# Optimization experiments

Hardware: AMD Instinct MI355X
Metric: run time of the kernel (lower is better)

## Reference

```python
import jax, jax.numpy as jnp
import numpy as np

# ---- constants derived from init kwargs ----
XB = (-30.0, 30.0, 0.15); YB = (-15.0, 15.0, 0.15)
NX = np.array([(XB[1]-XB[0])/XB[2], (YB[1]-YB[0])/YB[2]], np.float32)   # [400, 200]
DX = np.array([XB[2], YB[2]], np.float32)
BX = np.array([XB[0]+XB[2]/2.0, YB[0]+YB[2]/2.0], np.float32)
BOUND = DX/2.0 - BX                                                      # [30, 15]
CDIST_THR = float(np.linalg.norm(1.5/(2.0*BOUND)))
NUM_CLASSES = 3
B, N, G, PTS_PER_INS = 16, 1024, 1024, 32


def setup_inputs() -> dict:
    key = jax.random.key(0)
    k1, k2, k3, k4, k5 = jax.random.split(key, 5)
    # matches/semantics are log-probs (NLLLoss expects log-space inputs)
    matches = jax.nn.log_softmax(jax.random.normal(k1, (B, N+1, N+1), jnp.float32), axis=-1)
    positions = jax.random.uniform(k2, (B, N, 2), jnp.float32) * (jnp.asarray(NX) - 1.0)
    semantics = jax.nn.log_softmax(jax.random.normal(k3, (B, NUM_CLASSES, N), jnp.float32), axis=1)
    masks = jnp.ones((B, N, 1), jnp.float32)
    # raw GT points in metric coords in [-bound, bound]
    gt_pts = (jax.random.uniform(k4, (B, G, 2), jnp.float32) * 2.0 - 1.0) * jnp.asarray(BOUND)
    gt_ins = jnp.broadcast_to(jnp.arange(G, dtype=jnp.int32) // PTS_PER_INS, (B, G))
    gt_order = jnp.broadcast_to(jnp.arange(G, dtype=jnp.int32) % PTS_PER_INS, (B, G))
    gt_type = jax.random.randint(k5, (B, G), 0, NUM_CLASSES, dtype=jnp.int32)
    return {"matches": matches, "positions": positions, "semantics": semantics,
            "masks": masks, "gt_pts": gt_pts, "gt_ins": gt_ins,
            "gt_order": gt_order, "gt_type": gt_type}


def _per_sample(match, position, semantic, gt_pts, gt_ins, gt_order, gt_type):
    nx = jnp.asarray(NX, position.dtype)
    bound = jnp.asarray(BOUND, position.dtype)
    n = position.shape[0]
    pos = position / (nx - 1.0)                        # [N,2] normalized preds
    pgt = (gt_pts + bound) / (2.0 * bound)             # [G,2] normalized GT
    # cdist pred->gt, nearest GT per prediction
    cd = jnp.sqrt(jnp.sum((pos[:, None, :] - pgt[None, :, :])**2, -1) + 1e-12)  # [N,G]
    nearest = jnp.argmin(cd, 1)                        # [N]
    ndist = jnp.min(cd, 1)
    ins = jnp.where(ndist < CDIST_THR, gt_ins[nearest], -1)   # instance id or -1
    order = gt_order[nearest]
    # group preds by instance, sort by within-instance order (stable by index),
    # connect consecutive members: match_gt[prev, next] = 1
    perm = jnp.lexsort((jnp.arange(n), order, ins))    # primary key = ins
    a, b = perm[:-1], perm[1:]
    same = (ins[a] == ins[b]) & (ins[a] >= 0)
    M = jnp.zeros((n + 1, n + 1), match.dtype)
    M = M.at[a, b].add(same.astype(match.dtype))       # (a,b) pairs are unique
    # conflict resolution: each column keeps only the closest (in pred space) row
    dist_map = jnp.sqrt(jnp.sum((pos[:, None, :] - pos[None, :, :])**2, -1) + 1e-12)  # [N,N]
    blk = M[:n, :n]
    colsum = blk.sum(0)
    best = jnp.argmin(jnp.where(blk > 0, dist_map, jnp.inf), 0)             # [N]
    newblk = jax.nn.one_hot(best, n, dtype=match.dtype).T * (colsum > 0)    # [N,N]
    M = M.at[:n, :n].set(newblk)
    # dustbin assignments for unmatched rows/cols
    rowsum = M[:n, :].sum(1)
    M = M.at[:n, n].set((rowsum == 0).astype(match.dtype))
    colsum2 = M[:, :n].sum(0)
    M = M.at[n, :n].set((colsum2 == 0).astype(match.dtype))
    # NLL match losses (forward/backward direction), dustbin row/col excluded from targets
    t_back = jnp.argmax(M, 0)[:n]                      # per column: matched row
    t_fwd = jnp.argmax(M, 1)[:n]                       # per row: matched col
    j = jnp.arange(n)
    mloss = -jnp.mean(match[j, t_fwd]) - jnp.mean(match[j, t_back])
    # semantic gt from nearest GT type (no distance threshold, as in original)
    sem_cls = gt_type[nearest]                         # [N]
    sg = jax.nn.one_hot(sem_cls, NUM_CLASSES, dtype=semantic.dtype).T   # [C,N]
    semloss = -jnp.mean(semantic[sem_cls, j])
    closs = jnp.mean(jnp.abs(pos - pgt[nearest]))
    return closs, mloss, semloss, M, sg


def reference(matches, positions, semantics, masks, gt_pts, gt_ins, gt_order, gt_type):
    # masks assumed all-ones (full validity), so boolean compaction is identity
    closs, mloss, semloss, matches_gt, semantics_gt = jax.vmap(_per_sample)(
        matches, positions, semantics, gt_pts, gt_ins, gt_order, gt_type)
    return (jnp.mean(closs), jnp.mean(mloss), jnp.mean(semloss), matches_gt, semantics_gt)
```

## Files before the change

kernel.cpp:

```cpp
#include <hip/hip_runtime.h>
#include <math.h>

#define BB 16
#define NN 1024
#define GG 1024
#define NP1 1025
#define NC 3

__device__ __forceinline__ void get_consts(float& bnd0, float& bnd1,
                                           float& tb0, float& tb1, float& thr) {
    const float bx0 = (float)(-30.0 + 0.15 / 2.0);
    const float bx1 = (float)(-15.0 + 0.15 / 2.0);
    bnd0 = __fsub_rn(__fmul_rn(0.15f, 0.5f), bx0);
    bnd1 = __fsub_rn(__fmul_rn(0.15f, 0.5f), bx1);
    tb0 = __fmul_rn(2.0f, bnd0); tb1 = __fmul_rn(2.0f, bnd1);
    const float q0 = __fdiv_rn(1.5f, tb0), q1 = __fdiv_rn(1.5f, tb1);
    thr = __fsqrt_rn(__fadd_rn(__fmul_rn(q0, q0), __fmul_rn(q1, q1)));
}

__global__ void k_zero(float* __restrict__ out) {
    const long long idx = (long long)blockIdx.x * blockDim.x + threadIdx.x;
    const long long T   = (long long)gridDim.x * blockDim.x;
    float4* f4 = (float4*)(out + 4);
    const long long n4 = (16810000LL - 1) / 4;
    float4 z; z.x = 0.f; z.y = 0.f; z.z = 0.f; z.w = 0.f;
    for (long long k = idx; k < n4; k += T) f4[k] = z;
    if (idx == 0) {
        out[3] = 0.f;
        out[16810000] = 0.f; out[16810001] = 0.f; out[16810002] = 0.f;
    }
}

__global__ __launch_bounds__(128) void k_nearest1(
    const float* __restrict__ positions, const float* __restrict__ gt_pts,
    unsigned long long* __restrict__ part)
{
    __shared__ float2 sp[128];
    const int b = blockIdx.y;
    const int pc = blockIdx.x & 7, gs = blockIdx.x >> 3;
    const int tid = threadIdx.x;
    float bnd0, bnd1, tb0, tb1, thr;
    get_consts(bnd0, bnd1, tb0, tb1, thr);

    {
        const int g = (gs << 7) + tid;
        float2 gp = ((const float2*)gt_pts)[b * GG + g];
        float2 pg;
        pg.x = __fdiv_rn(__fadd_rn(gp.x, bnd0), tb0);
        pg.y = __fdiv_rn(__fadd_rn(gp.y, bnd1), tb1);
        sp[tid] = pg;
    }
    __syncthreads();

    const int i = (pc << 7) + tid;
    float2 p = ((const float2*)positions)[b * NN + i];
    const float px = __fdiv_rn(p.x, 399.0f);
    const float py = __fdiv_rn(p.y, 199.0f);

    unsigned long long best = ~0ull;
    const int gbase = gs << 7;
    #pragma unroll 8
    for (int g = 0; g < 128; ++g) {
        float2 pg = sp[g];
        float dx = __fsub_rn(px, pg.x);
        float dy = __fsub_rn(py, pg.y);
        float s  = __fadd_rn(__fadd_rn(__fmul_rn(dx, dx), __fmul_rn(dy, dy)), 1e-12f);
        float cd = __fsqrt_rn(s);
        unsigned long long pk =
            ((unsigned long long)__float_as_uint(cd) << 10) | (unsigned)(gbase + g);
        best = (pk < best) ? pk : best;
    }
    part[(((b << 3) + gs) << 10) + i] = best;
}

__global__ __launch_bounds__(128) void k_combine(
    const float* __restrict__ positions, const float* __restrict__ gt_pts,
    const int* __restrict__ gt_ins, const int* __restrict__ gt_order,
    const int* __restrict__ gt_type,
    const unsigned long long* __restrict__ part,
    int* __restrict__ key_ws, int* __restrict__ sem_ws,
    int* __restrict__ tf_ws, int* __restrict__ tb_ws,
    float* __restrict__ closs_part)
{
    __shared__ float red[128];
    const int b = blockIdx.y, pc = blockIdx.x, tid = threadIdx.x;
    const int i = (pc << 7) + tid;
    float bnd0, bnd1, tb0, tb1, thr;
    get_consts(bnd0, bnd1, tb0, tb1, thr);

    unsigned long long best = part[((b << 3) << 10) + i];
    #pragma unroll
    for (int gs = 1; gs < 8; ++gs) {
        unsigned long long v = part[(((b << 3) + gs) << 10) + i];
        best = (v < best) ? v : best;
    }
    const int bi = (int)(best & 1023u);
    const float cd = __uint_as_float((unsigned)(best >> 10));

    const int ins = (cd < thr) ? gt_ins[b * GG + bi] : -1;
    const int key = ((ins + 1) << 15) | (gt_order[b * GG + bi] << 10) | i;
    key_ws[(b << 10) + i] = key;
    sem_ws[(b << 10) + i] = gt_type[b * GG + bi];
    tf_ws[(b << 10) + i] = NN;
    tb_ws[(b << 10) + i] = NN;

    float2 p = ((const float2*)positions)[b * NN + i];
    const float px = __fdiv_rn(p.x, 399.0f);
    const float py = __fdiv_rn(p.y, 199.0f);
    float2 gp = ((const float2*)gt_pts)[b * GG + bi];
    const float pgx = __fdiv_rn(__fadd_rn(gp.x, bnd0), tb0);
    const float pgy = __fdiv_rn(__fadd_rn(gp.y, bnd1), tb1);
    const float cl = fabsf(__fsub_rn(px, pgx)) + fabsf(__fsub_rn(py, pgy));

    red[tid] = cl; __syncthreads();
    for (int s = 64; s > 0; s >>= 1) {
        if (tid < s) red[tid] += red[tid + s];
        __syncthreads();
    }
    if (tid == 0) closs_part[(b << 3) + pc] = red[0];
}

__global__ __launch_bounds__(128) void k_rank(
    const int* __restrict__ key_ws, int* __restrict__ sorted_ws)
{
    __shared__ int sk[NN];
    const int b = blockIdx.y, pc = blockIdx.x, tid = threadIdx.x;
    for (int j = tid; j < NN; j += 128) sk[j] = key_ws[(b << 10) + j];
    __syncthreads();
    const int k = sk[(pc << 7) + tid];
    int rank = 0;
    const int4* sk4 = (const int4*)sk;
    #pragma unroll 8
    for (int j = 0; j < 256; ++j) {
        int4 v = sk4[j];
        rank += (v.x < k) + (v.y < k) + (v.z < k) + (v.w < k);
    }
    sorted_ws[(b << 10) + rank] = k;
}

__global__ __launch_bounds__(128) void k_edges(
    const int* __restrict__ sorted_ws,
    int* __restrict__ tf_ws, int* __restrict__ tb_ws)
{
    const int b = blockIdx.y;
    const int p = (blockIdx.x << 7) + threadIdx.x;
    if (p >= NN - 1) return;
    const int k0 = sorted_ws[(b << 10) + p];
    const int k1 = sorted_ws[(b << 10) + p + 1];
    const int ia = (k0 >> 15) - 1;
    const int ic = (k1 >> 15) - 1;
    if (ia == ic && ia >= 0) {
        const int a = k0 & 1023, c = k1 & 1023;
        tf_ws[(b << 10) + a] = c;
        tb_ws[(b << 10) + c] = a;
    }
}

__global__ __launch_bounds__(128) void k_out(
    const float* __restrict__ matches, const float* __restrict__ semantics,
    const int* __restrict__ sem_ws,
    const int* __restrict__ tf_ws, const int* __restrict__ tb_ws,
    float* __restrict__ out, double* __restrict__ mpart, double* __restrict__ spart)
{
    __shared__ double redm[128], reds[128];
    const int b = blockIdx.y, pc = blockIdx.x, tid = threadIdx.x;
    const int i = (pc << 7) + tid;

    const int jf = tf_ws[(b << 10) + i];
    const int jb = tb_ws[(b << 10) + i];

    float* Mb = out + 3 + (size_t)b * NP1 * NP1;
    Mb[(size_t)i * NP1 + jf] = 1.0f;
    if (jb == NN) Mb[(size_t)NN * NP1 + i] = 1.0f;

    const float* mrow = matches + (size_t)b * NP1 * NP1 + (size_t)i * NP1;
    const double mp = (double)mrow[jf] + (double)mrow[jb];

    const int sc = sem_ws[(b << 10) + i];
    const double sv = (double)semantics[(b * NC + sc) * NN + i];

    float* sg = out + 3 + (size_t)BB * NP1 * NP1 + (size_t)b * NC * NN;
    sg[0 * NN + i] = (sc == 0) ? 1.0f : 0.0f;
    sg[1 * NN + i] = (sc == 1) ? 1.0f : 0.0f;
    sg[2 * NN + i] = (sc == 2) ? 1.0f : 0.0f;

    redm[tid] = mp; reds[tid] = sv; __syncthreads();
    for (int s = 64; s > 0; s >>= 1) {
        if (tid < s) { redm[tid] += redm[tid + s]; reds[tid] += reds[tid + s]; }
        __syncthreads();
    }
    if (tid == 0) { mpart[(b << 3) + pc] = redm[0]; spart[(b << 3) + pc] = reds[0]; }
}

__global__ __launch_bounds__(128) void k_final(
    const float* __restrict__ closs_part, const double* __restrict__ mpart,
    const double* __restrict__ spart, float* __restrict__ out)
{
    __shared__ double rc[128], rm[128], rs[128];
    const int t = threadIdx.x;
    rc[t] = (double)closs_part[t]; rm[t] = mpart[t]; rs[t] = spart[t];
    __syncthreads();
    for (int s = 64; s > 0; s >>= 1) {
        if (t < s) { rc[t] += rc[t + s]; rm[t] += rm[t + s]; rs[t] += rs[t + s]; }
        __syncthreads();
    }
    if (t == 0) {
        out[0] = (float)(rc[0] / 32768.0);
        out[1] = (float)(-rm[0] / 16384.0);
        out[2] = (float)(-rs[0] / 16384.0);
    }
}

extern "C" void kernel_launch(void* const* d_in, const int* in_sizes, int n_in,
                              void* d_out, int out_size, void* d_ws, size_t ws_size,
                              hipStream_t stream) {
    const float* matches   = (const float*)d_in[0];
    const float* positions = (const float*)d_in[1];
    const float* semantics = (const float*)d_in[2];
    const float* gt_pts    = (const float*)d_in[4];
    const int*   gt_ins    = (const int*)d_in[5];
    const int*   gt_order  = (const int*)d_in[6];
    const int*   gt_type   = (const int*)d_in[7];
    float* out = (float*)d_out;

    char* ws = (char*)d_ws;
    unsigned long long* part = (unsigned long long*)ws;
    int*    key_ws     = (int*)(ws + (1 << 20));
    int*    sem_ws     = (int*)(ws + (1 << 20) + (1 << 16));
    int*    sorted_ws  = (int*)(ws + (1 << 20) + (2 << 16));
    int*    tf_ws      = (int*)(ws + (1 << 20) + (3 << 16));
    int*    tb_ws      = (int*)(ws + (1 << 20) + (4 << 16));
    float*  closs_part = (float*)(ws + (1 << 20) + (5 << 16));
    double* mpart      = (double*)(ws + (1 << 20) + (5 << 16) + 1024);
    double* spart      = (double*)(ws + (1 << 20) + (5 << 16) + 2048);

    hipLaunchKernelGGL(k_zero,     dim3(2048),    dim3(256), 0, stream, out);
    hipLaunchKernelGGL(k_nearest1, dim3(64, 16),  dim3(128), 0, stream,
                       positions, gt_pts, part);
    hipLaunchKernelGGL(k_combine,  dim3(8, 16),   dim3(128), 0, stream,
                       positions, gt_pts, gt_ins, gt_order, gt_type, part,
                       key_ws, sem_ws, tf_ws, tb_ws, closs_part);
    hipLaunchKernelGGL(k_rank,     dim3(8, 16),   dim3(128), 0, stream, key_ws, sorted_ws);
    hipLaunchKernelGGL(k_edges,    dim3(8, 16),   dim3(128), 0, stream, sorted_ws, tf_ws, tb_ws);
    hipLaunchKernelGGL(k_out,      dim3(8, 16),   dim3(128), 0, stream,
                       matches, semantics, sem_ws, tf_ws, tb_ws, out, mpart, spart);
    hipLaunchKernelGGL(k_final,    dim3(1),       dim3(128), 0, stream,
                       closs_part, mpart, spart, out);
}
```

Baseline: 154.0 us.

## Fuse nearest search with combine and zero-fill output inside k_out

Merges the split nearest-GT search and its combine pass into one kernel that keeps all GT points in shared memory and reduces the eight partial minima in LDS. This removes the 64-bit partial buffer round trip and one launch. The separate whole-output zeroing kernel is dropped; each k_out block now zeroes its own 32 rows of M before scattering the ones, and writes the dustbin row explicitly. This folds the large memset into the scatter pass but adds a block barrier and smaller per-block work.

```diff
diff --git a/kernel.cpp b/kernel.cpp
--- a/kernel.cpp
+++ b/kernel.cpp
@@ -18,41 +18,31 @@
     thr = __fsqrt_rn(__fadd_rn(__fmul_rn(q0, q0), __fmul_rn(q1, q1)));
 }
 
-__global__ void k_zero(float* __restrict__ out) {
-    const long long idx = (long long)blockIdx.x * blockDim.x + threadIdx.x;
-    const long long T   = (long long)gridDim.x * blockDim.x;
-    float4* f4 = (float4*)(out + 4);
-    const long long n4 = (16810000LL - 1) / 4;
-    float4 z; z.x = 0.f; z.y = 0.f; z.z = 0.f; z.w = 0.f;
-    for (long long k = idx; k < n4; k += T) f4[k] = z;
-    if (idx == 0) {
-        out[3] = 0.f;
-        out[16810000] = 0.f; out[16810001] = 0.f; out[16810002] = 0.f;
-    }
-}
-
-__global__ __launch_bounds__(128) void k_nearest1(
+__global__ __launch_bounds__(512) void k_near(
     const float* __restrict__ positions, const float* __restrict__ gt_pts,
-    unsigned long long* __restrict__ part)
-{
-    __shared__ float2 sp[128];
-    const int b = blockIdx.y;
-    const int pc = blockIdx.x & 7, gs = blockIdx.x >> 3;
-    const int tid = threadIdx.x;
+    const int* __restrict__ gt_ins, const int* __restrict__ gt_order,
+    const int* __restrict__ gt_type,
+    int* __restrict__ key_ws, int* __restrict__ sem_ws,
+    int* __restrict__ tf_ws, int* __restrict__ tb_ws,
+    float* __restrict__ closs_part)
+{
+    __shared__ float2 sp[GG];
+    __shared__ unsigned long long pl[512];
+    const int b = blockIdx.y, pc = blockIdx.x, tid = threadIdx.x;
+    const int sub = tid & 63, gs = tid >> 6;
     float bnd0, bnd1, tb0, tb1, thr;
     get_consts(bnd0, bnd1, tb0, tb1, thr);
 
-    {
-        const int g = (gs << 7) + tid;
+    for (int g = tid; g < GG; g += 512) {
         float2 gp = ((const float2*)gt_pts)[b * GG + g];
         float2 pg;
         pg.x = __fdiv_rn(__fadd_rn(gp.x, bnd0), tb0);
         pg.y = __fdiv_rn(__fadd_rn(gp.y, bnd1), tb1);
-        sp[tid] = pg;
-    }
-    __syncthreads();
-
-    const int i = (pc << 7) + tid;
+        sp[g] = pg;
+    }
+    __syncthreads();
+
+    const int i = (pc << 6) + sub;
     float2 p = ((const float2*)positions)[b * NN + i];
     const float px = __fdiv_rn(p.x, 399.0f);
     const float py = __fdiv_rn(p.y, 199.0f);
@@ -60,64 +50,45 @@
     unsigned long long best = ~0ull;
     const int gbase = gs << 7;
     #pragma unroll 8
-    for (int g = 0; g < 128; ++g) {
-        float2 pg = sp[g];
+    for (int j = 0; j < 128; ++j) {
+        float2 pg = sp[gbase + j];
         float dx = __fsub_rn(px, pg.x);
         float dy = __fsub_rn(py, pg.y);
         float s  = __fadd_rn(__fadd_rn(__fmul_rn(dx, dx), __fmul_rn(dy, dy)), 1e-12f);
         float cd = __fsqrt_rn(s);
         unsigned long long pk =
-            ((unsigned long long)__float_as_uint(cd) << 10) | (unsigned)(gbase + g);
+            ((unsigned long long)__float_as_uint(cd) << 10) | (unsigned)(gbase + j);
         best = (pk < best) ? pk : best;
     }
-    part[(((b << 3) + gs) << 10) + i] = best;
-}
-
-__global__ __launch_bounds__(128) void k_combine(
-    const float* __restrict__ positions, const float* __restrict__ gt_pts,
-    const int* __restrict__ gt_ins, const int* __restrict__ gt_order,
-    const int* __restrict__ gt_type,
-    const unsigned long long* __restrict__ part,
-    int* __restrict__ key_ws, int* __restrict__ sem_ws,
-    int* __restrict__ tf_ws, int* __restrict__ tb_ws,
-    float* __restrict__ closs_part)
-{
-    __shared__ float red[128];
-    const int b = blockIdx.y, pc = blockIdx.x, tid = threadIdx.x;
-    const int i = (pc << 7) + tid;
-    float bnd0, bnd1, tb0, tb1, thr;
-    get_consts(bnd0, bnd1, tb0, tb1, thr);
-
-    unsigned long long best = part[((b << 3) << 10) + i];
+    pl[tid] = best;
+    __syncthreads();
     #pragma unroll
-    for (int gs = 1; gs < 8; ++gs) {
-        unsigned long long v = part[(((b << 3) + gs) << 10) + i];
-        best = (v < best) ? v : best;
-    }
-    const int bi = (int)(best & 1023u);
-    const float cd = __uint_as_float((unsigned)(best >> 10));
-
-    const int ins = (cd < thr) ? gt_ins[b * GG + bi] : -1;
-    const int key = ((ins + 1) << 15) | (gt_order[b * GG + bi] << 10) | i;
-    key_ws[(b << 10) + i] = key;
-    sem_ws[(b << 10) + i] = gt_type[b * GG + bi];
-    tf_ws[(b << 10) + i] = NN;
-    tb_ws[(b << 10) + i] = NN;
-
-    float2 p = ((const float2*)positions)[b * NN + i];
-    const float px = __fdiv_rn(p.x, 399.0f);
-    const float py = __fdiv_rn(p.y, 199.0f);
-    float2 gp = ((const float2*)gt_pts)[b * GG + bi];
-    const float pgx = __fdiv_rn(__fadd_rn(gp.x, bnd0), tb0);
-    const float pgy = __fdiv_rn(__fadd_rn(gp.y, bnd1), tb1);
-    const float cl = fabsf(__fsub_rn(px, pgx)) + fabsf(__fsub_rn(py, pgy));
-
-    red[tid] = cl; __syncthreads();
-    for (int s = 64; s > 0; s >>= 1) {
-        if (tid < s) red[tid] += red[tid + s];
+    for (int s = 4; s > 0; s >>= 1) {
+        if (gs < s) {
+            unsigned long long v = pl[tid + (s << 6)];
+            if (v < pl[tid]) pl[tid] = v;
+        }
         __syncthreads();
     }
-    if (tid == 0) closs_part[(b << 3) + pc] = red[0];
+
+    if (tid < 64) {
+        best = pl[tid];
+        const int bi = (int)(best & 1023u);
+        const float cd = __uint_as_float((unsigned)(best >> 10));
+
+        const int ins = (cd < thr) ? gt_ins[b * GG + bi] : -1;
+        const int key = ((ins + 1) << 15) | (gt_order[b * GG + bi] << 10) | i;
+        key_ws[(b << 10) + i] = key;
+        sem_ws[(b << 10) + i] = gt_type[b * GG + bi];
+        tf_ws[(b << 10) + i] = NN;
+        tb_ws[(b << 10) + i] = NN;
+
+        float2 pg = sp[bi];
+        float cl = fabsf(__fsub_rn(px, pg.x)) + fabsf(__fsub_rn(py, pg.y));
+        #pragma unroll
+        for (int s = 32; s > 0; s >>= 1) cl += __shfl_down(cl, s);
+        if (tid == 0) closs_part[(b << 4) + pc] = cl;
+    }
 }
 
 __global__ __launch_bounds__(128) void k_rank(
@@ -138,12 +109,12 @@
     sorted_ws[(b << 10) + rank] = k;
 }
 
-__global__ __launch_bounds__(128) void k_edges(
+__global__ __launch_bounds__(512) void k_edges(
     const int* __restrict__ sorted_ws,
     int* __restrict__ tf_ws, int* __restrict__ tb_ws)
 {
     const int b = blockIdx.y;
-    const int p = (blockIdx.x << 7) + threadIdx.x;
+    const int p = (blockIdx.x << 9) + threadIdx.x;
     if (p >= NN - 1) return;
     const int k0 = sorted_ws[(b << 10) + p];
     const int k1 = sorted_ws[(b << 10) + p + 1];
@@ -156,51 +127,74 @@
     }
 }
 
-__global__ __launch_bounds__(128) void k_out(
+__global__ __launch_bounds__(256) void k_out(
     const float* __restrict__ matches, const float* __restrict__ semantics,
     const int* __restrict__ sem_ws,
     const int* __restrict__ tf_ws, const int* __restrict__ tb_ws,
     float* __restrict__ out, double* __restrict__ mpart, double* __restrict__ spart)
 {
-    __shared__ double redm[128], reds[128];
     const int b = blockIdx.y, pc = blockIdx.x, tid = threadIdx.x;
-    const int i = (pc << 7) + tid;
-
-    const int jf = tf_ws[(b << 10) + i];
-    const int jb = tb_ws[(b << 10) + i];
-
     float* Mb = out + 3 + (size_t)b * NP1 * NP1;
-    Mb[(size_t)i * NP1 + jf] = 1.0f;
-    if (jb == NN) Mb[(size_t)NN * NP1 + i] = 1.0f;
-
-    const float* mrow = matches + (size_t)b * NP1 * NP1 + (size_t)i * NP1;
-    const double mp = (double)mrow[jf] + (double)mrow[jb];
-
-    const int sc = sem_ws[(b << 10) + i];
-    const double sv = (double)semantics[(b * NC + sc) * NN + i];
-
-    float* sg = out + 3 + (size_t)BB * NP1 * NP1 + (size_t)b * NC * NN;
-    sg[0 * NN + i] = (sc == 0) ? 1.0f : 0.0f;
-    sg[1 * NN + i] = (sc == 1) ? 1.0f : 0.0f;
-    sg[2 * NN + i] = (sc == 2) ? 1.0f : 0.0f;
-
-    redm[tid] = mp; reds[tid] = sv; __syncthreads();
-    for (int s = 64; s > 0; s >>= 1) {
-        if (tid < s) { redm[tid] += redm[tid + s]; reds[tid] += reds[tid + s]; }
-        __syncthreads();
-    }
-    if (tid == 0) { mpart[(b << 3) + pc] = redm[0]; spart[(b << 3) + pc] = reds[0]; }
-}
-
-__global__ __launch_bounds__(128) void k_final(
+
+    {
+        float* base = Mb + (size_t)pc * 32 * NP1;
+        const int total = 32 * NP1;
+        const int mis = (int)(((size_t)base >> 2) & 3);
+        const int head = (4 - mis) & 3;
+        const int n4 = (total - head) >> 2;
+        const int tail = total - head - (n4 << 2);
+        if (tid < head) base[tid] = 0.f;
+        float4* b4 = (float4*)(base + head);
+        float4 z; z.x = 0.f; z.y = 0.f; z.z = 0.f; z.w = 0.f;
+        for (int k = tid; k < n4; k += 256) b4[k] = z;
+        if (tid < tail) base[head + (n4 << 2) + tid] = 0.f;
+    }
+    __syncthreads();
+
+    if (tid < 64) {
+        double mv = 0.0, sv = 0.0;
+        if (tid < 32) {
+            const int i = (pc << 5) + tid;
+            const int jf = tf_ws[(b << 10) + i];
+            const int jb = tb_ws[(b << 10) + i];
+
+            Mb[(size_t)i * NP1 + jf] = 1.0f;
+            Mb[(size_t)NN * NP1 + i] = (jb == NN) ? 1.0f : 0.0f;
+            if (pc == 0 && tid == 0) Mb[(size_t)NN * NP1 + NN] = 0.f;
+
+            const float* mrow = matches + (size_t)b * NP1 * NP1 + (size_t)i * NP1;
+            mv = (double)mrow[jf] + (double)mrow[jb];
+
+            const int sc = sem_ws[(b << 10) + i];
+            sv = (double)semantics[(b * NC + sc) * NN + i];
+
+            float* sg = out + 3 + (size_t)BB * NP1 * NP1 + (size_t)b * NC * NN;
+            sg[0 * NN + i] = (sc == 0) ? 1.0f : 0.0f;
+            sg[1 * NN + i] = (sc == 1) ? 1.0f : 0.0f;
+            sg[2 * NN + i] = (sc == 2) ? 1.0f : 0.0f;
+        }
+        #pragma unroll
+        for (int s = 32; s > 0; s >>= 1) {
+            mv += __shfl_down(mv, s);
+            sv += __shfl_down(sv, s);
+        }
+        if (tid == 0) {
+            mpart[(b << 5) + pc] = mv;
+            spart[(b << 5) + pc] = sv;
+        }
+    }
+}
+
+__global__ __launch_bounds__(512) void k_final(
     const float* __restrict__ closs_part, const double* __restrict__ mpart,
     const double* __restrict__ spart, float* __restrict__ out)
 {
-    __shared__ double rc[128], rm[128], rs[128];
+    __shared__ double rc[512], rm[512], rs[512];
     const int t = threadIdx.x;
-    rc[t] = (double)closs_part[t]; rm[t] = mpart[t]; rs[t] = spart[t];
-    __syncthreads();
-    for (int s = 64; s > 0; s >>= 1) {
+    rc[t] = (t < 256) ? (double)closs_part[t] : 0.0;
+    rm[t] = mpart[t]; rs[t] = spart[t];
+    __syncthreads();
+    for (int s = 256; s > 0; s >>= 1) {
         if (t < s) { rc[t] += rc[t + s]; rm[t] += rm[t + s]; rs[t] += rs[t + s]; }
         __syncthreads();
     }
@@ -224,26 +218,22 @@
     float* out = (float*)d_out;
 
     char* ws = (char*)d_ws;
-    unsigned long long* part = (unsigned long long*)ws;
-    int*    key_ws     = (int*)(ws + (1 << 20));
-    int*    sem_ws     = (int*)(ws + (1 << 20) + (1 << 16));
-    int*    sorted_ws  = (int*)(ws + (1 << 20) + (2 << 16));
-    int*    tf_ws      = (int*)(ws + (1 << 20) + (3 << 16));
-    int*    tb_ws      = (int*)(ws + (1 << 20) + (4 << 16));
-    float*  closs_part = (float*)(ws + (1 << 20) + (5 << 16));
-    double* mpart      = (double*)(ws + (1 << 20) + (5 << 16) + 1024);
-    double* spart      = (double*)(ws + (1 << 20) + (5 << 16) + 2048);
-
-    hipLaunchKernelGGL(k_zero,     dim3(2048),    dim3(256), 0, stream, out);
-    hipLaunchKernelGGL(k_nearest1, dim3(64, 16),  dim3(128), 0, stream,
-                       positions, gt_pts, part);
-    hipLaunchKernelGGL(k_combine,  dim3(8, 16),   dim3(128), 0, stream,
-                       positions, gt_pts, gt_ins, gt_order, gt_type, part,
+    int*    key_ws     = (int*)(ws + 0 * 65536);
+    int*    sem_ws     = (int*)(ws + 1 * 65536);
+    int*    sorted_ws  = (int*)(ws + 2 * 65536);
+    int*    tf_ws      = (int*)(ws + 3 * 65536);
+    int*    tb_ws      = (int*)(ws + 4 * 65536);
+    float*  closs_part = (float*)(ws + 5 * 65536);
+    double* mpart      = (double*)(ws + 5 * 65536 + 4096);
+    double* spart      = (double*)(ws + 5 * 65536 + 8192);
+
+    hipLaunchKernelGGL(k_near,  dim3(16, 16), dim3(512), 0, stream,
+                       positions, gt_pts, gt_ins, gt_order, gt_type,
                        key_ws, sem_ws, tf_ws, tb_ws, closs_part);
-    hipLaunchKernelGGL(k_rank,     dim3(8, 16),   dim3(128), 0, stream, key_ws, sorted_ws);
-    hipLaunchKernelGGL(k_edges,    dim3(8, 16),   dim3(128), 0, stream, sorted_ws, tf_ws, tb_ws);
-    hipLaunchKernelGGL(k_out,      dim3(8, 16),   dim3(128), 0, stream,
+    hipLaunchKernelGGL(k_rank,  dim3(8, 16),  dim3(128), 0, stream, key_ws, sorted_ws);
+    hipLaunchKernelGGL(k_edges, dim3(2, 16),  dim3(512), 0, stream, sorted_ws, tf_ws, tb_ws);
+    hipLaunchKernelGGL(k_out,   dim3(32, 16), dim3(256), 0, stream,
                        matches, semantics, sem_ws, tf_ws, tb_ws, out, mpart, spart);
-    hipLaunchKernelGGL(k_final,    dim3(1),       dim3(128), 0, stream,
+    hipLaunchKernelGGL(k_final, dim3(1),      dim3(512), 0, stream,
                        closs_part, mpart, spart, out);
 }
```

Measured after the change: 148.9 us. -3.3%, faster.
